# Performance work log

Measured on AMD Instinct MI355X. Metric: run time of the kernel, lower is better.

Reference implementation:

```python
import jax, jax.numpy as jnp
import numpy as np

B, C, H, W = 4, 512, 128, 128
CQ = C // 8  # in_dim // reduction


def setup_inputs() -> dict:
    key = jax.random.key(0)
    ks = jax.random.split(key, 8)
    s = 1.0 / np.sqrt(C)
    return {
        "x": jax.random.normal(ks[0], (B, C, H, W), jnp.float32),
        "Wq": jax.random.normal(ks[1], (CQ, C), jnp.float32) * s,
        "bq": jax.random.normal(ks[2], (CQ,), jnp.float32) * 0.01,
        "Wk": jax.random.normal(ks[3], (CQ, C), jnp.float32) * s,
        "bk": jax.random.normal(ks[4], (CQ,), jnp.float32) * 0.01,
        "Wv": jax.random.normal(ks[5], (C, C), jnp.float32) * s,
        "bv": jax.random.normal(ks[6], (C,), jnp.float32) * 0.01,
        "gamma": jax.random.uniform(ks[7], (1,), jnp.float32) * 0.1,
    }


def reference(x, Wq, bq, Wk, bk, Wv, bv, gamma):
    b, c, h, w = x.shape
    cq = Wq.shape[0]
    # 1x1 convs == per-pixel GEMMs
    q = jnp.einsum('bchw,oc->bohw', x, Wq) + bq[None, :, None, None]
    k = jnp.einsum('bchw,oc->bohw', x, Wk) + bk[None, :, None, None]
    v = jnp.einsum('bchw,oc->bohw', x, Wv) + bv[None, :, None, None]

    # --- horizontal (row) attention ---
    qh = jnp.transpose(q, (0, 2, 3, 1)).reshape(b * h, w, cq)      # (BH, W, Cq)
    # faithful to torch .view(): raw reshape of (W,Cq) block -> (Cq,W), NOT a transpose
    kh = jnp.transpose(k, (0, 2, 3, 1)).reshape(b * h, cq, w)      # (BH, Cq, W)
    vh = jnp.transpose(v, (0, 2, 3, 1)).reshape(b * h, w, c)       # (BH, W, C)
    ah = jax.nn.softmax(jnp.matmul(qh, kh), axis=-1)               # (BH, W, W)
    ch = jnp.matmul(ah, vh).reshape(b, h, w, c).transpose(0, 3, 1, 2)

    # --- vertical (column) attention ---
    qv = jnp.transpose(q, (0, 3, 1, 2)).reshape(b * w, h, cq)      # faithful raw reshape of (Cq,H) -> (H,Cq)
    kv = jnp.transpose(k, (0, 3, 1, 2)).reshape(b * w, cq, h)      # (BW, Cq, H)
    vv = jnp.transpose(v, (0, 3, 1, 2)).reshape(b * w, h, c)       # faithful raw reshape
    av = jax.nn.softmax(jnp.matmul(qv, kv), axis=-1)               # (BW, H, H)
    cv = jnp.matmul(av, vv).reshape(b, w, h, c).transpose(0, 3, 2, 1)

    return gamma * (ch + cv) + x
```

## Files before the change

kernel.cpp:

```cpp
#include <hip/hip_runtime.h>
#include <stdint.h>

#define B_ 4
#define C_ 512
#define CQ_ 64
#define H_ 128
#define W_ 128
#define HW_ 16384

typedef unsigned short u16;
typedef unsigned int u32;
typedef __attribute__((ext_vector_type(8))) __bf16 bf16x8;
typedef __attribute__((ext_vector_type(4))) float f32x4;

union BF8 { bf16x8 v; u16 s[8]; u32 u[4]; uint4 q4; };

__device__ __forceinline__ u16 f2bf(float f) {
    u32 v; __builtin_memcpy(&v, &f, 4);
    v = (v + 0x7FFFu + ((v >> 16) & 1u)) >> 16;
    return (u16)v;
}
__device__ __forceinline__ float bf2f(u16 a) {
    u32 v = ((u32)a) << 16; float f; __builtin_memcpy(&f, &v, 4); return f;
}

#define WS_XT  0u
#define WS_CV  0u
#define WS_Q   33554432u
#define WS_K   37748736u
#define WS_V   41943040u
#define WS_QT  75497472u
#define WS_KT  79691776u
#define WS_WB  75497472u
#define WS_VT  83886080u

__global__ __launch_bounds__(256) void prep_x(const float* __restrict__ x, u16* __restrict__ ws)
{
    __shared__ __align__(16) u16 tl[64][72];
    const int t = threadIdx.x;
    const int pt = blockIdx.x, ct = blockIdx.y, b = blockIdx.z;
    const int p0 = pt * 64, c0 = ct * 64;
    const float* xb = x + ((u32)(b*C_ + c0))*HW_ + p0;
    #pragma unroll
    for (int pass = 0; pass < 4; ++pass) {
        int ci = pass*256 + t, cl = ci >> 4, p4 = ci & 15;
        float4 d = *reinterpret_cast<const float4*>(xb + (u32)cl*HW_ + p4*4);
        tl[p4*4+0][cl] = f2bf(d.x); tl[p4*4+1][cl] = f2bf(d.y);
        tl[p4*4+2][cl] = f2bf(d.z); tl[p4*4+3][cl] = f2bf(d.w);
    }
    __syncthreads();
    u16* dst = ws + WS_XT + ((u32)((b<<14) + p0))*512 + c0;
    #pragma unroll
    for (int pass = 0; pass < 2; ++pass) {
        int ci = pass*256 + t, pr = ci >> 3, k8 = ci & 7;
        uint4 d = *reinterpret_cast<const uint4*>(&tl[pr][k8*8]);
        *reinterpret_cast<uint4*>(dst + (u32)pr*512 + k8*8) = d;
    }
}

__global__ __launch_bounds__(256) void prep_w(const float* __restrict__ Wq, const float* __restrict__ Wk,
                                              const float* __restrict__ Wv, u16* __restrict__ ws)
{
    const int f = (blockIdx.x*256 + threadIdx.x)*4;
    const float* src;
    if (f < 32768)      src = Wq + f;
    else if (f < 65536) src = Wk + (f - 32768);
    else                src = Wv + (f - 65536);
    float4 d = *reinterpret_cast<const float4*>(src);
    u16 e[4] = { f2bf(d.x), f2bf(d.y), f2bf(d.z), f2bf(d.w) };
    *reinterpret_cast<uint2*>(ws + WS_WB + f) = *reinterpret_cast<const uint2*>(e);
}

__global__ __launch_bounds__(256) void proj_kernel(const float* __restrict__ bq, const float* __restrict__ bk,
                                                   const float* __restrict__ bv, u16* __restrict__ ws)
{
    __shared__ __align__(16) u16 As[128][72];
    __shared__ __align__(16) u16 Bs[128][72];
    const int t = threadIdx.x;
    const int bm = blockIdx.x, bn = blockIdx.y, b = blockIdx.z;
    const int m0 = bm*128, p0 = bn*128;
    const u16* WB = ws + WS_WB;
    const u16* XT = ws + WS_XT + ((u32)((b<<14) + p0))*512;
    const int wv = t >> 6, ln = t & 63, quad = ln >> 4, col = ln & 15;
    const int mh = (wv>>1)*64, nh = (wv&1)*64;

    f32x4 acc[4][4];
    #pragma unroll
    for (int mt = 0; mt < 4; ++mt)
        #pragma unroll
        for (int nt = 0; nt < 4; ++nt) acc[mt][nt] = (f32x4){0.f,0.f,0.f,0.f};

    for (int c0 = 0; c0 < 512; c0 += 64) {
        #pragma unroll
        for (int pass = 0; pass < 4; ++pass) {
            int ci = pass*256 + t, row = ci >> 3, k8 = ci & 7;
            uint4 da = *reinterpret_cast<const uint4*>(WB + (u32)(m0+row)*512 + c0 + k8*8);
            *reinterpret_cast<uint4*>(&As[row][k8*8]) = da;
            uint4 db = *reinterpret_cast<const uint4*>(XT + (u32)row*512 + c0 + k8*8);
            *reinterpret_cast<uint4*>(&Bs[row][k8*8]) = db;
        }
        __syncthreads();
        #pragma unroll
        for (int ks = 0; ks < 2; ++ks) {
            const int kk = ks*32 + quad*8;
            bf16x8 am[4], bn_[4];
            #pragma unroll
            for (int mt = 0; mt < 4; ++mt) am[mt]  = *reinterpret_cast<const bf16x8*>(&As[mh + mt*16 + col][kk]);
            #pragma unroll
            for (int nt = 0; nt < 4; ++nt) bn_[nt] = *reinterpret_cast<const bf16x8*>(&Bs[nh + nt*16 + col][kk]);
            #pragma unroll
            for (int mt = 0; mt < 4; ++mt)
                #pragma unroll
                for (int nt = 0; nt < 4; ++nt)
                    acc[mt][nt] = __builtin_amdgcn_mfma_f32_16x16x32_bf16(am[mt], bn_[nt], acc[mt][nt], 0, 0, 0);
        }
        __syncthreads();
    }
    const int h = bn;
    #pragma unroll
    for (int mt = 0; mt < 4; ++mt) {
        const int obase = m0 + mh + mt*16 + quad*4;
        #pragma unroll
        for (int r = 0; r < 4; ++r) {
            const int o = obase + r;
            float bb; u16* dst;
            if (o < 64)       { bb = bq[o];     dst = ws + WS_Q + ((u32)((b<<6) + o))*HW_ + p0; }
            else if (o < 128) { bb = bk[o-64];  dst = ws + WS_K + ((u32)((b<<6) + (o-64)))*HW_ + p0; }
            else              { bb = bv[o-128]; dst = ws + WS_V + (u32)b*8388608u + (u32)h*65536u + (u32)(o-128)*128u; }
            #pragma unroll
            for (int nt = 0; nt < 4; ++nt) {
                int pl = nh + nt*16 + col;
                dst[pl] = f2bf(acc[mt][nt][r] + bb);
            }
        }
    }
}

__global__ __launch_bounds__(256) void transpose_qk(u16* __restrict__ ws)
{
    __shared__ u16 tl[64][70];
    const int t = threadIdx.x;
    const int tile = blockIdx.x, img = blockIdx.y;
    const int h0 = (tile >> 1) * 64, w0 = (tile & 1) * 64;
    const u16* src = ws + WS_Q + (u32)img * HW_;
    u16* dst = ws + WS_QT + (u32)img * HW_;
    #pragma unroll
    for (int pass = 0; pass < 2; ++pass) {
        int ci = pass*256 + t, hl = ci >> 3, w8 = ci & 7;
        uint4 d = *reinterpret_cast<const uint4*>(src + (u32)(h0+hl)*W_ + w0 + w8*8);
        const u16* e = reinterpret_cast<const u16*>(&d);
        #pragma unroll
        for (int j = 0; j < 8; ++j) tl[w8*8+j][hl] = e[j];
    }
    __syncthreads();
    #pragma unroll
    for (int pass = 0; pass < 4; ++pass) {
        int ci = pass*256 + t, wl = ci >> 4, h4 = ci & 15;
        uint2 d;
        d.x = *reinterpret_cast<const u32*>(&tl[wl][h4*4]);
        d.y = *reinterpret_cast<const u32*>(&tl[wl][h4*4+2]);
        *reinterpret_cast<uint2*>(dst + (u32)(w0+wl)*H_ + h0 + h4*4) = d;
    }
}

__global__ __launch_bounds__(256) void transpose_v(u16* __restrict__ ws)
{
    __shared__ u16 tl[64][70];
    const int t = threadIdx.x;
    const int tile = blockIdx.x, c = blockIdx.y, b = blockIdx.z;
    const int h0 = (tile >> 1) * 64, w0 = (tile & 1) * 64;
    const u16* src = ws + WS_V + (u32)b*8388608u + (u32)c*128u;
    u16* dst = ws + WS_VT + (u32)b*8388608u + (u32)c*16384u;
    #pragma unroll
    for (int pass = 0; pass < 2; ++pass) {
        int ci = pass*256 + t, hl = ci >> 3, w8 = ci & 7;
        uint4 d = *reinterpret_cast<const uint4*>(src + (u32)(h0+hl)*65536u + w0 + w8*8);
        const u16* e = reinterpret_cast<const u16*>(&d);
        #pragma unroll
        for (int j = 0; j < 8; ++j) tl[w8*8+j][hl] = e[j];
    }
    __syncthreads();
    #pragma unroll
    for (int pass = 0; pass < 4; ++pass) {
        int ci = pass*256 + t, wl = ci >> 4, h4 = ci & 15;
        uint2 d;
        d.x = *reinterpret_cast<const u32*>(&tl[wl][h4*4]);
        d.y = *reinterpret_cast<const u32*>(&tl[wl][h4*4+2]);
        *reinterpret_cast<uint2*>(dst + (u32)(w0+wl)*128u + h0 + h4*4) = d;
    }
}

union __align__(16) ShAttn {
    struct QK { u16 q[128][72]; u16 kt[128][72]; } qk;
    u16 a[128][136];
};

__global__ __launch_bounds__(256) void hattn_kernel(const u16* __restrict__ ws, float* __restrict__ outp)
{
    __shared__ ShAttn sh;
    const int t = threadIdx.x;
    const int h = blockIdx.x, b = blockIdx.y;
    const u16* qsrc = ws + WS_Q + (u32)(b*CQ_)*HW_ + h*W_;
    const u16* ksrc = ws + WS_K + (u32)(b*CQ_)*HW_ + h*W_;

    for (int e = t; e < 8192; e += 256) {
        int cq = e >> 7, w = e & 127;
        sh.qk.q[w][cq] = qsrc[cq*HW_ + w];
        u16 kv = ksrc[cq*HW_ + w];
        sh.qk.kt[cq + ((w & 1) << 6)][w >> 1] = kv;
    }
    __syncthreads();

    const int wv = t >> 6, ln = t & 63, quad = ln >> 4, col = ln & 15;
    f32x4 accs[2][8];
    #pragma unroll
    for (int mt = 0; mt < 2; ++mt)
        #pragma unroll
        for (int nt = 0; nt < 8; ++nt) accs[mt][nt] = (f32x4){0.f,0.f,0.f,0.f};

    #pragma unroll
    for (int ks = 0; ks < 2; ++ks) {
        bf16x8 bfv[8];
        #pragma unroll
        for (int nt = 0; nt < 8; ++nt)
            bfv[nt] = *reinterpret_cast<const bf16x8*>(&sh.qk.kt[nt*16 + col][ks*32 + quad*8]);
        #pragma unroll
        for (int mt = 0; mt < 2; ++mt) {
            bf16x8 af = *reinterpret_cast<const bf16x8*>(&sh.qk.q[(wv*2 + mt)*16 + col][ks*32 + quad*8]);
            #pragma unroll
            for (int nt = 0; nt < 8; ++nt)
                accs[mt][nt] = __builtin_amdgcn_mfma_f32_16x16x32_bf16(af, bfv[nt], accs[mt][nt], 0, 0, 0);
        }
    }
    #pragma unroll
    for (int mt = 0; mt < 2; ++mt) {
        #pragma unroll
        for (int r = 0; r < 4; ++r) {
            float mx = accs[mt][0][r];
            #pragma unroll
            for (int nt = 1; nt < 8; ++nt) mx = fmaxf(mx, accs[mt][nt][r]);
            #pragma unroll
            for (int d = 1; d <= 8; d <<= 1) mx = fmaxf(mx, __shfl_xor(mx, d, 64));
            float sum = 0.f;
            #pragma unroll
            for (int nt = 0; nt < 8; ++nt) { float ev = __expf(accs[mt][nt][r] - mx); accs[mt][nt][r] = ev; sum += ev; }
            #pragma unroll
            for (int d = 1; d <= 8; d <<= 1) sum += __shfl_xor(sum, d, 64);
            float inv = 1.f / sum;
            #pragma unroll
            for (int nt = 0; nt < 8; ++nt) accs[mt][nt][r] *= inv;
        }
    }
    __syncthreads();
    #pragma unroll
    for (int mt = 0; mt < 2; ++mt)
        #pragma unroll
        for (int nt = 0; nt < 8; ++nt)
            #pragma unroll
            for (int r = 0; r < 4; ++r) {
                int w1 = (wv*2 + mt)*16 + quad*4 + r;
                int w2 = nt*16 + col;
                sh.a[w1][w2] = f2bf(accs[mt][nt][r]);
            }
    __syncthreads();

    const u16* vsrc = ws + WS_V + (u32)b*8388608u + (u32)h*65536u;
    float* chout = outp + (u32)(b*C_)*HW_ + h*W_;
    const int ccw = wv * 128;
    for (int mp = 0; mp < 4; ++mp) {
        f32x4 accv[2][8];
        #pragma unroll
        for (int mi = 0; mi < 2; ++mi)
            #pragma unroll
            for (int nt = 0; nt < 8; ++nt) accv[mi][nt] = (f32x4){0.f,0.f,0.f,0.f};
        #pragma unroll
        for (int ks = 0; ks < 4; ++ks) {
            bf16x8 bfv[8];
            #pragma unroll
            for (int nt = 0; nt < 8; ++nt)
                bfv[nt] = *reinterpret_cast<const bf16x8*>(&sh.a[nt*16 + col][ks*32 + quad*8]);
            #pragma unroll
            for (int mi = 0; mi < 2; ++mi) {
                int cct = ccw + (mp*2 + mi)*16;
                bf16x8 af = *reinterpret_cast<const bf16x8*>(&vsrc[(u32)(cct + col)*128u + ks*32 + quad*8]);
                #pragma unroll
                for (int nt = 0; nt < 8; ++nt)
                    accv[mi][nt] = __builtin_amdgcn_mfma_f32_16x16x32_bf16(af, bfv[nt], accv[mi][nt], 0, 0, 0);
            }
        }
        #pragma unroll
        for (int mi = 0; mi < 2; ++mi)
            #pragma unroll
            for (int nt = 0; nt < 8; ++nt)
                #pragma unroll
                for (int r = 0; r < 4; ++r) {
                    int cc = ccw + (mp*2 + mi)*16 + quad*4 + r;
                    int w1 = nt*16 + col;
                    chout[(u32)cc*HW_ + w1] = accv[mi][nt][r];
                }
    }
}

union __align__(16) ShV {
    struct QK { u16 q[128][72]; u16 kt[128][72]; } qk;
    struct PV { u16 a[128][136]; u16 vld[128][144]; } pv;
};

__global__ __launch_bounds__(256) void vattn_kernel(u16* __restrict__ ws)
{
    __shared__ ShV sh;
    const int t = threadIdx.x;
    const int w = blockIdx.x, b = blockIdx.y;
    const u16* qTs = ws + WS_QT + (u32)(b*CQ_)*HW_ + w*H_;
    const u16* kTs = ws + WS_KT + (u32)(b*CQ_)*HW_ + w*H_;

    for (int e = t; e < 8192; e += 256) {
        int cq = e >> 7, hh = e & 127;
        sh.qk.q[2*cq + (hh >> 6)][hh & 63] = qTs[cq*HW_ + hh];
        sh.qk.kt[hh][cq] = kTs[cq*HW_ + hh];
    }
    __syncthreads();

    const int wv = t >> 6, ln = t & 63, quad = ln >> 4, col = ln & 15;
    f32x4 accs[2][8];
    #pragma unroll
    for (int mt = 0; mt < 2; ++mt)
        #pragma unroll
        for (int nt = 0; nt < 8; ++nt) accs[mt][nt] = (f32x4){0.f,0.f,0.f,0.f};

    #pragma unroll
    for (int ks = 0; ks < 2; ++ks) {
        bf16x8 bfv[8];
        #pragma unroll
        for (int nt = 0; nt < 8; ++nt)
            bfv[nt] = *reinterpret_cast<const bf16x8*>(&sh.qk.kt[nt*16 + col][ks*32 + quad*8]);
        #pragma unroll
        for (int mt = 0; mt < 2; ++mt) {
            bf16x8 af = *reinterpret_cast<const bf16x8*>(&sh.qk.q[(wv*2 + mt)*16 + col][ks*32 + quad*8]);
            #pragma unroll
            for (int nt = 0; nt < 8; ++nt)
                accs[mt][nt] = __builtin_amdgcn_mfma_f32_16x16x32_bf16(af, bfv[nt], accs[mt][nt], 0, 0, 0);
        }
    }
    #pragma unroll
    for (int mt = 0; mt < 2; ++mt) {
        #pragma unroll
        for (int r = 0; r < 4; ++r) {
            float mx = accs[mt][0][r];
            #pragma unroll
            for (int nt = 1; nt < 8; ++nt) mx = fmaxf(mx, accs[mt][nt][r]);
            #pragma unroll
            for (int d = 1; d <= 8; d <<= 1) mx = fmaxf(mx, __shfl_xor(mx, d, 64));
            float sum = 0.f;
            #pragma unroll
            for (int nt = 0; nt < 8; ++nt) { float ev = __expf(accs[mt][nt][r] - mx); accs[mt][nt][r] = ev; sum += ev; }
            #pragma unroll
            for (int d = 1; d <= 8; d <<= 1) sum += __shfl_xor(sum, d, 64);
            float inv = 1.f / sum;
            #pragma unroll
            for (int nt = 0; nt < 8; ++nt) accs[mt][nt][r] *= inv;
        }
    }
    __syncthreads();
    #pragma unroll
    for (int mt = 0; mt < 2; ++mt)
        #pragma unroll
        for (int nt = 0; nt < 8; ++nt)
            #pragma unroll
            for (int r = 0; r < 4; ++r) {
                int h1 = (wv*2 + mt)*16 + quad*4 + r;
                int h2 = nt*16 + col;
                sh.pv.a[h1][h2] = f2bf(accs[mt][nt][r]);
            }
    __syncthreads();

    const u32 vtb = WS_VT + (u32)b*8388608u + (u32)w*128u;
    u16* cvout = ws + WS_CV + (u32)(b*C_)*HW_ + (u32)w*H_;
    for (int mp = 0; mp < 4; ++mp) {
        if (mp) __syncthreads();
        #pragma unroll
        for (int pass = 0; pass < 8; ++pass) {
            int ci = pass*256 + t, h2 = ci >> 4, kj = ci & 15;
            uint4 d = *reinterpret_cast<const uint4*>(ws + vtb + (u32)(4*h2 + mp)*16384u + kj*8);
            *reinterpret_cast<uint4*>(&sh.pv.vld[h2][kj*8]) = d;
        }
        __syncthreads();
        f32x4 accv[2][8];
        #pragma unroll
        for (int mi = 0; mi < 2; ++mi)
            #pragma unroll
            for (int nt = 0; nt < 8; ++nt) accv[mi][nt] = (f32x4){0.f,0.f,0.f,0.f};
        #pragma unroll
        for (int ks = 0; ks < 4; ++ks) {
            bf16x8 bfv[8];
            #pragma unroll
            for (int nt = 0; nt < 8; ++nt)
                bfv[nt] = *reinterpret_cast<const bf16x8*>(&sh.pv.a[nt*16 + col][ks*32 + quad*8]);
            #pragma unroll
            for (int mi = 0; mi < 2; ++mi) {
                const int clo = wv*32 + mi*16;
                BF8 af;
                #pragma unroll
                for (int jj = 0; jj < 8; ++jj)
                    af.s[jj] = sh.pv.vld[ks*32 + quad*8 + jj][clo + col];
                #pragma unroll
                for (int nt = 0; nt < 8; ++nt)
                    accv[mi][nt] = __builtin_amdgcn_mfma_f32_16x16x32_bf16(af.v, bfv[nt], accv[mi][nt], 0, 0, 0);
            }
        }
        #pragma unroll
        for (int mi = 0; mi < 2; ++mi)
            #pragma unroll
            for (int nt = 0; nt < 8; ++nt)
                #pragma unroll
                for (int r = 0; r < 4; ++r) {
                    int cc = mp*128 + wv*32 + mi*16 + quad*4 + r;
                    int h1 = nt*16 + col;
                    cvout[(u32)cc*HW_ + h1] = f2bf(accv[mi][nt][r]);
                }
    }
}

__global__ __launch_bounds__(256) void combine_kernel(const u16* __restrict__ ws, const float* __restrict__ x,
                                                      const float* __restrict__ gamma, float* __restrict__ outp)
{
    __shared__ u16 tl[64][70];
    const int t = threadIdx.x;
    const int tile = blockIdx.x, cc = blockIdx.y, b = blockIdx.z;
    const int h0 = (tile >> 1) * 64, w0 = (tile & 1) * 64;
    const float g = gamma[0];
    const u32 base = ((u32)(b*C_) + cc) * HW_;
    const u16* cvs = ws + WS_CV + base;
    #pragma unroll
    for (int pass = 0; pass < 2; ++pass) {
        int ci = pass*256 + t, wl = ci >> 3, h8 = ci & 7;
        uint4 d = *reinterpret_cast<const uint4*>(cvs + (u32)(w0+wl)*H_ + h0 + h8*8);
        const u16* e = reinterpret_cast<const u16*>(&d);
        #pragma unroll
        for (int j = 0; j < 8; ++j) tl[h8*8+j][wl] = e[j];
    }
    __syncthreads();
    #pragma unroll
    for (int pass = 0; pass < 4; ++pass) {
        int ci = pass*256 + t, hl = ci >> 4, w4 = ci & 15;
        u32 idx = base + (u32)(h0+hl)*W_ + w0 + w4*4;
        u32 p0 = *reinterpret_cast<const u32*>(&tl[hl][w4*4]);
        u32 p1 = *reinterpret_cast<const u32*>(&tl[hl][w4*4+2]);
        float4 ch = *reinterpret_cast<const float4*>(outp + idx);
        float4 xx = *reinterpret_cast<const float4*>(x + idx);
        float4 o;
        o.x = g*(ch.x + bf2f((u16)p0))         + xx.x;
        o.y = g*(ch.y + bf2f((u16)(p0 >> 16))) + xx.y;
        o.z = g*(ch.z + bf2f((u16)p1))         + xx.z;
        o.w = g*(ch.w + bf2f((u16)(p1 >> 16))) + xx.w;
        *reinterpret_cast<float4*>(outp + idx) = o;
    }
}

extern "C" void kernel_launch(void* const* d_in, const int* in_sizes, int n_in,
                              void* d_out, int out_size, void* d_ws, size_t ws_size,
                              hipStream_t stream)
{
    const float* x  = (const float*)d_in[0];
    const float* Wq = (const float*)d_in[1];
    const float* bq = (const float*)d_in[2];
    const float* Wk = (const float*)d_in[3];
    const float* bk = (const float*)d_in[4];
    const float* Wv = (const float*)d_in[5];
    const float* bv = (const float*)d_in[6];
    const float* gm = (const float*)d_in[7];
    float* out = (float*)d_out;
    u16* ws  = (u16*)d_ws;

    prep_x<<<dim3(256, 8, 4), 256, 0, stream>>>(x, ws);
    prep_w<<<dim3(320), 256, 0, stream>>>(Wq, Wk, Wv, ws);
    proj_kernel<<<dim3(5, 128, 4), 256, 0, stream>>>(bq, bk, bv, ws);
    transpose_qk<<<dim3(4, 512), 256, 0, stream>>>(ws);
    transpose_v<<<dim3(4, 512, 4), 256, 0, stream>>>(ws);
    hattn_kernel<<<dim3(128, 4), 256, 0, stream>>>(ws, out);
    vattn_kernel<<<dim3(128, 4), 256, 0, stream>>>(ws);
    combine_kernel<<<dim3(4, 512, 4), 256, 0, stream>>>(ws, x, gm, out);
}
```

Before: 594.4 us.

## Shuffle V into per-column MFMA-ready layout and read A-fragments directly from global

Replaces the V transpose kernel with a shuffle that writes V in a per-(b,w) layout where each channel row holds 128 contiguous h values, with the faithful raw-reshape permutation applied in the shuffle. The vertical attention kernel then loads its MFMA A-operand as one 16-byte vector straight from global memory. This removes the per-mp LDS staging of V, its syncthreads, and the 8 scalar strided LDS reads per fragment. The risk is that global fragment loads are uncoalesced across lanes and are no longer shared through LDS, and the shuffle kernel does scalar gathers from LDS.

```diff
diff --git a/kernel.cpp b/kernel.cpp
--- a/kernel.cpp
+++ b/kernel.cpp
@@ -12,8 +12,6 @@
 typedef unsigned int u32;
 typedef __attribute__((ext_vector_type(8))) __bf16 bf16x8;
 typedef __attribute__((ext_vector_type(4))) float f32x4;
-
-union BF8 { bf16x8 v; u16 s[8]; u32 u[4]; uint4 q4; };
 
 __device__ __forceinline__ u16 f2bf(float f) {
     u32 v; __builtin_memcpy(&v, &f, 4);
@@ -163,30 +161,31 @@
     }
 }
 
-__global__ __launch_bounds__(256) void transpose_v(u16* __restrict__ ws)
-{
-    __shared__ u16 tl[64][70];
-    const int t = threadIdx.x;
-    const int tile = blockIdx.x, c = blockIdx.y, b = blockIdx.z;
-    const int h0 = (tile >> 1) * 64, w0 = (tile & 1) * 64;
-    const u16* src = ws + WS_V + (u32)b*8388608u + (u32)c*128u;
-    u16* dst = ws + WS_VT + (u32)b*8388608u + (u32)c*16384u;
-    #pragma unroll
-    for (int pass = 0; pass < 2; ++pass) {
-        int ci = pass*256 + t, hl = ci >> 3, w8 = ci & 7;
-        uint4 d = *reinterpret_cast<const uint4*>(src + (u32)(h0+hl)*65536u + w0 + w8*8);
-        const u16* e = reinterpret_cast<const u16*>(&d);
-        #pragma unroll
-        for (int j = 0; j < 8; ++j) tl[w8*8+j][hl] = e[j];
-    }
-    __syncthreads();
-    #pragma unroll
-    for (int pass = 0; pass < 4; ++pass) {
-        int ci = pass*256 + t, wl = ci >> 4, h4 = ci & 15;
-        uint2 d;
-        d.x = *reinterpret_cast<const u32*>(&tl[wl][h4*4]);
-        d.y = *reinterpret_cast<const u32*>(&tl[wl][h4*4+2]);
-        *reinterpret_cast<uint2*>(dst + (u32)(w0+wl)*128u + h0 + h4*4) = d;
+__global__ __launch_bounds__(256) void shuffle_v(u16* __restrict__ ws)
+{
+    __shared__ u16 tl[128][134];
+    const int t = threadIdx.x;
+    const int ct = blockIdx.x, h = blockIdx.y, b = blockIdx.z;
+    const int c0 = ct * 128;
+    const u16* src = ws + WS_V + (u32)b*8388608u + (u32)h*65536u + (u32)c0*128u;
+    #pragma unroll
+    for (int pass = 0; pass < 8; ++pass) {
+        int ci = pass*256 + t, cl = ci >> 4, w8 = ci & 15;
+        uint4 d = *reinterpret_cast<const uint4*>(src + (u32)cl*128u + w8*8);
+        *reinterpret_cast<uint4*>(&tl[cl][w8*8]) = d;
+    }
+    __syncthreads();
+    u16* dst = ws + WS_VT + (u32)b*8388608u;
+    #pragma unroll
+    for (int pass = 0; pass < 8; ++pass) {
+        int ci = pass*256 + t;
+        int w = ci >> 4, g = (ci >> 2) & 3, q4 = ci & 3;
+        u16 e[8];
+        #pragma unroll
+        for (int jj = 0; jj < 8; ++jj)
+            e[jj] = tl[4*(q4*8 + jj) + g][w];
+        *reinterpret_cast<uint4*>(dst + (u32)w*65536u + (u32)(g*128 + h)*128u + (c0>>2) + q4*8)
+            = *reinterpret_cast<const uint4*>(e);
     }
 }
 
@@ -303,7 +302,7 @@
 
 union __align__(16) ShV {
     struct QK { u16 q[128][72]; u16 kt[128][72]; } qk;
-    struct PV { u16 a[128][136]; u16 vld[128][144]; } pv;
+    u16 a[128][136];
 };
 
 __global__ __launch_bounds__(256) void vattn_kernel(u16* __restrict__ ws)
@@ -370,21 +369,13 @@
             for (int r = 0; r < 4; ++r) {
                 int h1 = (wv*2 + mt)*16 + quad*4 + r;
                 int h2 = nt*16 + col;
-                sh.pv.a[h1][h2] = f2bf(accs[mt][nt][r]);
+                sh.a[h1][h2] = f2bf(accs[mt][nt][r]);
             }
     __syncthreads();
 
-    const u32 vtb = WS_VT + (u32)b*8388608u + (u32)w*128u;
+    const u16* vvs = ws + WS_VT + ((u32)(b*W_ + w))*65536u;
     u16* cvout = ws + WS_CV + (u32)(b*C_)*HW_ + (u32)w*H_;
     for (int mp = 0; mp < 4; ++mp) {
-        if (mp) __syncthreads();
-        #pragma unroll
-        for (int pass = 0; pass < 8; ++pass) {
-            int ci = pass*256 + t, h2 = ci >> 4, kj = ci & 15;
-            uint4 d = *reinterpret_cast<const uint4*>(ws + vtb + (u32)(4*h2 + mp)*16384u + kj*8);
-            *reinterpret_cast<uint4*>(&sh.pv.vld[h2][kj*8]) = d;
-        }
-        __syncthreads();
         f32x4 accv[2][8];
         #pragma unroll
         for (int mi = 0; mi < 2; ++mi)
@@ -395,17 +386,14 @@
             bf16x8 bfv[8];
             #pragma unroll
             for (int nt = 0; nt < 8; ++nt)
-                bfv[nt] = *reinterpret_cast<const bf16x8*>(&sh.pv.a[nt*16 + col][ks*32 + quad*8]);
+                bfv[nt] = *reinterpret_cast<const bf16x8*>(&sh.a[nt*16 + col][ks*32 + quad*8]);
             #pragma unroll
             for (int mi = 0; mi < 2; ++mi) {
-                const int clo = wv*32 + mi*16;
-                BF8 af;
-                #pragma unroll
-                for (int jj = 0; jj < 8; ++jj)
-                    af.s[jj] = sh.pv.vld[ks*32 + quad*8 + jj][clo + col];
+                int ccrow = mp*128 + wv*32 + mi*16 + col;
+                bf16x8 af = *reinterpret_cast<const bf16x8*>(&vvs[(u32)ccrow*128u + ks*32 + quad*8]);
                 #pragma unroll
                 for (int nt = 0; nt < 8; ++nt)
-                    accv[mi][nt] = __builtin_amdgcn_mfma_f32_16x16x32_bf16(af.v, bfv[nt], accv[mi][nt], 0, 0, 0);
+                    accv[mi][nt] = __builtin_amdgcn_mfma_f32_16x16x32_bf16(af, bfv[nt], accv[mi][nt], 0, 0, 0);
             }
         }
         #pragma unroll
@@ -476,7 +464,7 @@
     prep_w<<<dim3(320), 256, 0, stream>>>(Wq, Wk, Wv, ws);
     proj_kernel<<<dim3(5, 128, 4), 256, 0, stream>>>(bq, bk, bv, ws);
     transpose_qk<<<dim3(4, 512), 256, 0, stream>>>(ws);
-    transpose_v<<<dim3(4, 512, 4), 256, 0, stream>>>(ws);
+    shuffle_v<<<dim3(4, 128, 4), 256, 0, stream>>>(ws);
     hattn_kernel<<<dim3(128, 4), 256, 0, stream>>>(ws, out);
     vattn_kernel<<<dim3(128, 4), 256, 0, stream>>>(ws);
     combine_kernel<<<dim3(4, 512, 4), 256, 0, stream>>>(ws, x, gm, out);
```

Result: faster. 580.8 us (-2.3%).
